# Kernel tuning notes

Hardware: AMD Instinct MI355X
Metric: run time of the kernel (lower is better)

Reference implementation:

```python
import jax, jax.numpy as jnp
import numpy as np

NUM_HEADS = 32
MICRO_BATCHES = 2
TOP_K = 2
LN_EPS = 1e-5


def _mha(x, scale, bias, wq, wk, wv, wo):
    # Pre-LN multi-head self-attention with residual (RealSelfAttention).
    B, S, D = x.shape
    H = NUM_HEADS
    hd = D // H
    res = x
    mu = jnp.mean(x, axis=-1, keepdims=True)
    xc = x - mu
    var = jnp.mean(xc * xc, axis=-1, keepdims=True)
    xn = xc / jnp.sqrt(var + LN_EPS) * scale + bias
    q = (xn @ wq.T).reshape(B, S, H, hd).transpose(0, 2, 1, 3)
    k = (xn @ wk.T).reshape(B, S, H, hd).transpose(0, 2, 1, 3)
    v = (xn @ wv.T).reshape(B, S, H, hd).transpose(0, 2, 1, 3)
    scores = jnp.einsum('bhqd,bhkd->bhqk', q, k) * (1.0 / np.sqrt(hd).astype(np.float32))
    attn = jax.nn.softmax(scores, axis=-1)
    o = jnp.einsum('bhqk,bhkd->bhqd', attn, v).transpose(0, 2, 1, 3).reshape(B, S, D)
    return o @ wo.T + res


def setup_inputs() -> dict:
    key = jax.random.key(0)
    D, E, F = 1024, 8, 4096
    B, S = 4, 1024
    ks = jax.random.split(key, 16)
    w = lambda k, shape: (jax.random.normal(k, shape, dtype=jnp.float32) * 0.02)
    return {
        'x': jax.random.normal(ks[0], (B, S, D), dtype=jnp.float32),
        'ln1_scale': jnp.ones((D,), jnp.float32),
        'ln1_bias': jnp.zeros((D,), jnp.float32),
        'wq1': w(ks[1], (D, D)), 'wk1': w(ks[2], (D, D)),
        'wv1': w(ks[3], (D, D)), 'wo1': w(ks[4], (D, D)),
        'gate_w': w(ks[5], (E, D)),
        'exp_w1': w(ks[6], (E, F, D)), 'exp_b1': jnp.zeros((E, F), jnp.float32),
        'exp_w2': w(ks[7], (E, D, F)), 'exp_b2': jnp.zeros((E, D), jnp.float32),
        'ln2_scale': jnp.ones((D,), jnp.float32),
        'ln2_bias': jnp.zeros((D,), jnp.float32),
        'wq2': w(ks[8], (D, D)), 'wk2': w(ks[9], (D, D)),
        'wv2': w(ks[10], (D, D)), 'wo2': w(ks[11], (D, D)),
    }


def reference(x, ln1_scale, ln1_bias, wq1, wk1, wv1, wo1, gate_w,
              exp_w1, exp_b1, exp_w2, exp_b2,
              ln2_scale, ln2_bias, wq2, wk2, wv2, wo2):
    B, S, D = x.shape
    E = exp_w1.shape[0]
    # PreOps: attention layer L (per-sample, so full-batch apply == per-microbatch apply)
    y = _mha(x, ln1_scale, ln1_bias, wq1, wk1, wv1, wo1)
    # Gate: logits + top-k indices computed in source but never applied to tokens.
    flat = y.reshape(B * S, D)
    logits = flat @ gate_w.T
    _ = jax.lax.top_k(logits, TOP_K)  # indices unused downstream (faithful to source)
    # Dispatch (all_to_all on 1 device == identity): per-microbatch flat tokens are
    # chunked equally across local experts.
    T = (B // MICRO_BATCHES) * S            # tokens per microbatch
    toks = y.reshape(MICRO_BATCHES, E, T // E, D)
    h = jax.nn.gelu(jnp.einsum('metd,efd->metf', toks, exp_w1) + exp_b1[None, :, None, :],
                    approximate=False)
    eo = jnp.einsum('metf,edf->metd', h, exp_w2) + exp_b2[None, :, None, :]
    # Combine (identity) + PostOps: attention layer L+1
    z = eo.reshape(B, S, D)
    out = _mha(z, ln2_scale, ln2_bias, wq2, wk2, wv2, wo2)
    return out
```

## Files before the change

kernel.cpp:

```cpp
#include <hip/hip_runtime.h>

typedef __attribute__((ext_vector_type(8))) short bf16x8;
typedef __attribute__((ext_vector_type(4))) float f32x4;
typedef __attribute__((ext_vector_type(4))) short short4v;

#define DEV __device__ __forceinline__

DEV short f2bf(float f) {
  union { float f; unsigned u; } x; x.f = f;
  unsigned r = x.u + 0x7fffu + ((x.u >> 16) & 1u);
  return (short)(r >> 16);
}

#define GL2LDS16(g, l) __builtin_amdgcn_global_load_lds(                      \
    (const __attribute__((address_space(1))) void*)(g),                       \
    (__attribute__((address_space(3))) void*)(l), 16, 0, 0)

__global__ __launch_bounds__(256) void k_cast_bf16(const float* __restrict__ s,
                                                   short* __restrict__ d, int n4) {
  int i = blockIdx.x * 256 + threadIdx.x;
  if (i >= n4) return;
  float4 v = ((const float4*)s)[i];
  short4v o;
  o[0] = f2bf(v.x); o[1] = f2bf(v.y); o[2] = f2bf(v.z); o[3] = f2bf(v.w);
  ((short4v*)d)[i] = o;
}

__global__ __launch_bounds__(256)
void k_ln(const float* __restrict__ X, const float* __restrict__ G,
          const float* __restrict__ Bi, short* __restrict__ Y) {
  const int row = blockIdx.x, t = threadIdx.x;
  const float4 v = ((const float4*)(X + (size_t)row * 1024))[t];
  float s = v.x + v.y + v.z + v.w;
  float s2 = v.x * v.x + v.y * v.y + v.z * v.z + v.w * v.w;
#pragma unroll
  for (int m = 1; m < 64; m <<= 1) { s += __shfl_xor(s, m); s2 += __shfl_xor(s2, m); }
  __shared__ float rs[4], rq[4];
  const int w = t >> 6, lane = t & 63;
  if (lane == 0) { rs[w] = s; rq[w] = s2; }
  __syncthreads();
  s = rs[0] + rs[1] + rs[2] + rs[3];
  s2 = rq[0] + rq[1] + rq[2] + rq[3];
  const float mu = s * (1.f / 1024.f);
  const float var = s2 * (1.f / 1024.f) - mu * mu;
  const float rstd = rsqrtf(var + 1e-5f);
  const float4 g = ((const float4*)G)[t];
  const float4 bi = ((const float4*)Bi)[t];
  short4v o;
  o[0] = f2bf((v.x - mu) * rstd * g.x + bi.x);
  o[1] = f2bf((v.y - mu) * rstd * g.y + bi.y);
  o[2] = f2bf((v.z - mu) * rstd * g.z + bi.z);
  o[3] = f2bf((v.w - mu) * rstd * g.w + bi.w);
  ((short4v*)(Y + (size_t)row * 1024))[t] = o;
}

template <int EPI, int EXPERT>
__global__ __launch_bounds__(256)
void k_gemm_bt(const short* __restrict__ A, const short* __restrict__ Bt,
               void* __restrict__ Cv, const float* __restrict__ Res,
               const float* __restrict__ Bias, int M, int N, int K) {
  __shared__ __attribute__((aligned(16))) short As[128 * 32];
  __shared__ __attribute__((aligned(16))) short Bs[128 * 32];
  const int tid = threadIdx.x;
  const int w = tid >> 6, lane = tid & 63;
  const int r16 = lane & 15, kg = lane >> 4;
  const int wr = w >> 1, wc = w & 1;

  size_t rowBase = (size_t)blockIdx.y * 128;
  size_t bOff = 0, biasOff = 0;
  if constexpr (EXPERT) {
    int e = blockIdx.z >> 1, mb = blockIdx.z & 1;
    rowBase += (size_t)(mb * 8 + e) * 256;
    bOff = (size_t)e * N * K;
    biasOff = (size_t)e * N;
  }
  const size_t col0 = (size_t)blockIdx.x * 128;
  const short* Ab = A + rowBase * K;
  const short* Bb = Bt + bOff + col0 * K;

  f32x4 acc[4][4] = {};

  for (int k0 = 0; k0 < K; k0 += 32) {
    __syncthreads();
#pragma unroll
    for (int i = 0; i < 2; ++i) {
      int c = (i * 4 + w) * 64 + lane;
      int row = c >> 2;
      int sl = (c & 3) ^ (row & 3);
      GL2LDS16(Ab + (size_t)row * K + k0 + sl * 8, (char*)As + (size_t)(i * 4 + w) * 1024);
      GL2LDS16(Bb + (size_t)row * K + k0 + sl * 8, (char*)Bs + (size_t)(i * 4 + w) * 1024);
    }
    __syncthreads();
    bf16x8 af[4], bg[4];
#pragma unroll
    for (int m = 0; m < 4; ++m) {
      int row = wr * 64 + m * 16 + r16;
      af[m] = *(const bf16x8*)(As + row * 32 + (kg ^ (row & 3)) * 8);
    }
#pragma unroll
    for (int n = 0; n < 4; ++n) {
      int row = wc * 64 + n * 16 + r16;
      bg[n] = *(const bf16x8*)(Bs + row * 32 + (kg ^ (row & 3)) * 8);
    }
#pragma unroll
    for (int m = 0; m < 4; ++m)
#pragma unroll
      for (int n = 0; n < 4; ++n)
        acc[m][n] = __builtin_amdgcn_mfma_f32_16x16x32_bf16(af[m], bg[n], acc[m][n], 0, 0, 0);
  }

#pragma unroll
  for (int m = 0; m < 4; ++m) {
    size_t grow0 = rowBase + wr * 64 + m * 16 + kg * 4;
#pragma unroll
    for (int n = 0; n < 4; ++n) {
      size_t gcol = col0 + wc * 64 + n * 16 + r16;
#pragma unroll
      for (int r = 0; r < 4; ++r) {
        size_t idx = (grow0 + r) * (size_t)N + gcol;
        float v = acc[m][n][r];
        if constexpr (EPI == 1 || EPI == 4) v += Res[idx];
        if constexpr (EPI == 2 || EPI == 3) v += Bias[biasOff + gcol];
        if constexpr (EPI == 2) v = 0.5f * v * (1.f + erff(v * 0.70710678118654752f));
        if constexpr (EPI <= 2) ((short*)Cv)[idx] = f2bf(v);
        else                    ((float*)Cv)[idx] = v;
      }
    }
  }
}

__global__ __launch_bounds__(256, 3)
void k_attn(const short* __restrict__ QKV, short* __restrict__ O) {
  const int qt = blockIdx.x, h = blockIdx.y, b = blockIdx.z;
  const int tid = threadIdx.x, w = tid >> 6, lane = tid & 63;
  const int r16 = lane & 15, kg = lane >> 4;

  __shared__ __attribute__((aligned(16))) short Kl[2][128 * 32];
  __shared__ __attribute__((aligned(16))) short Vt[2][32 * 128];
  __shared__ __attribute__((aligned(16))) short Pl[4][16 * 128];

  const size_t tb = (size_t)b * 1024;
  const int qbase = qt * 128 + w * 32;

  bf16x8 aq[2];
#pragma unroll
  for (int f = 0; f < 2; ++f)
    aq[f] = *(const bf16x8*)(QKV + (tb + qbase + f * 16 + r16) * 3072 + h * 32 + kg * 8);

  f32x4 acc[2][2] = {};
  float lreg[2][4] = {};
  const float scale = 0.17677669529663687f;

  auto stageK = [&](int bid, int kc) {
#pragma unroll
    for (int i = 0; i < 2; ++i) {
      int c = (i * 4 + w) * 64 + lane;
      int row = c >> 2;
      int sl = (c & 3) ^ (row & 3);
      GL2LDS16(QKV + (tb + kc * 128 + row) * 3072 + 1024 + h * 32 + sl * 8,
               (char*)Kl[bid] + (size_t)(i * 4 + w) * 1024);
    }
  };

  stageK(0, 0);
  {
    int c0 = tid,        vr0 = c0 >> 2, d00 = (c0 & 3) * 8;
    int c1 = 256 + tid,  vr1 = c1 >> 2, d01 = (c1 & 3) * 8;
    bf16x8 v0 = *(const bf16x8*)(QKV + (tb + vr0) * 3072 + 2048 + h * 32 + d00);
    bf16x8 v1 = *(const bf16x8*)(QKV + (tb + vr1) * 3072 + 2048 + h * 32 + d01);
#pragma unroll
    for (int j = 0; j < 8; ++j) {
      int da = d00 + j, db = d01 + j;
      Vt[0][((da * 128 + vr0) ^ ((da & 7) << 3))] = v0[j];
      Vt[0][((db * 128 + vr1) ^ ((db & 7) << 3))] = v1[j];
    }
  }
  __syncthreads();

  int bi = 0;
  for (int kc = 0; kc < 8; ++kc) {
    bf16x8 nv0, nv1;
    int nvr0 = 0, nd0 = 0, nvr1 = 0, nd1 = 0;
    if (kc < 7) {
      stageK(bi ^ 1, kc + 1);
      const short* Vg = QKV + (tb + (size_t)(kc + 1) * 128) * 3072 + 2048 + h * 32;
      int c0 = tid;       nvr0 = c0 >> 2; nd0 = (c0 & 3) * 8;
      int c1 = 256 + tid; nvr1 = c1 >> 2; nd1 = (c1 & 3) * 8;
      nv0 = *(const bf16x8*)(Vg + (size_t)nvr0 * 3072 + nd0);
      nv1 = *(const bf16x8*)(Vg + (size_t)nvr1 * 3072 + nd1);
    }

    f32x4 s[2][8];
#pragma unroll
    for (int kt = 0; kt < 8; ++kt) {
      int row = kt * 16 + r16;
      bf16x8 bk = *(const bf16x8*)(Kl[bi] + row * 32 + (kg ^ (row & 3)) * 8);
      f32x4 zz = {0.f, 0.f, 0.f, 0.f};
      s[0][kt] = __builtin_amdgcn_mfma_f32_16x16x32_bf16(aq[0], bk, zz, 0, 0, 0);
      s[1][kt] = __builtin_amdgcn_mfma_f32_16x16x32_bf16(aq[1], bk, zz, 0, 0, 0);
    }

#pragma unroll
    for (int f = 0; f < 2; ++f)
#pragma unroll
      for (int r = 0; r < 4; ++r) {
        float sum = 0.f;
#pragma unroll
        for (int kt = 0; kt < 8; ++kt) {
          float p = __expf(s[f][kt][r] * scale);
          s[f][kt][r] = p;
          sum += p;
        }
#pragma unroll
        for (int m = 1; m < 16; m <<= 1) sum += __shfl_xor(sum, m);
        lreg[f][r] += sum;
      }

    short* P = Pl[w];
#pragma unroll
    for (int f = 0; f < 2; ++f) {
#pragma unroll
      for (int kt = 0; kt < 8; ++kt)
#pragma unroll
        for (int r = 0; r < 4; ++r) {
          int row = kg * 4 + r;
          P[((row * 128 + kt * 16 + r16) ^ ((row & 7) << 3))] = f2bf(s[f][kt][r]);
        }
#pragma unroll
      for (int ks = 0; ks < 4; ++ks) {
        bf16x8 pa = *(const bf16x8*)(P + ((r16 * 128 + ks * 32 + kg * 8) ^ ((r16 & 7) << 3)));
#pragma unroll
        for (int dt = 0; dt < 2; ++dt) {
          int vrow = dt * 16 + r16;
          bf16x8 bv = *(const bf16x8*)(Vt[bi] + ((vrow * 128 + ks * 32 + kg * 8) ^ ((vrow & 7) << 3)));
          acc[f][dt] = __builtin_amdgcn_mfma_f32_16x16x32_bf16(pa, bv, acc[f][dt], 0, 0, 0);
        }
      }
    }

    if (kc < 7) {
#pragma unroll
      for (int j = 0; j < 8; ++j) {
        int da = nd0 + j, db = nd1 + j;
        Vt[bi ^ 1][((da * 128 + nvr0) ^ ((da & 7) << 3))] = nv0[j];
        Vt[bi ^ 1][((db * 128 + nvr1) ^ ((db & 7) << 3))] = nv1[j];
      }
    }

    __syncthreads();
    bi ^= 1;
  }

#pragma unroll
  for (int f = 0; f < 2; ++f)
#pragma unroll
    for (int r = 0; r < 4; ++r) {
      float inv = 1.f / lreg[f][r];
      size_t qrow = tb + qbase + f * 16 + kg * 4 + r;
#pragma unroll
      for (int dt = 0; dt < 2; ++dt)
        O[qrow * 1024 + h * 32 + dt * 16 + r16] = f2bf(acc[f][dt][r] * inv);
    }
}

extern "C" void kernel_launch(void* const* d_in, const int* in_sizes, int n_in,
                              void* d_out, int out_size, void* d_ws, size_t ws_size,
                              hipStream_t stream) {
  const float* x    = (const float*)d_in[0];
  const float* ln1s = (const float*)d_in[1];
  const float* ln1b = (const float*)d_in[2];
  const float* wq1  = (const float*)d_in[3];
  const float* wk1  = (const float*)d_in[4];
  const float* wv1  = (const float*)d_in[5];
  const float* wo1  = (const float*)d_in[6];
  const float* ew1  = (const float*)d_in[8];
  const float* eb1  = (const float*)d_in[9];
  const float* ew2  = (const float*)d_in[10];
  const float* eb2  = (const float*)d_in[11];
  const float* ln2s = (const float*)d_in[12];
  const float* ln2b = (const float*)d_in[13];
  const float* wq2  = (const float*)d_in[14];
  const float* wk2  = (const float*)d_in[15];
  const float* wv2  = (const float*)d_in[16];
  const float* wo2  = (const float*)d_in[17];

  char* ws = (char*)d_ws;
  size_t off = 0;
  auto alloc = [&](size_t bytes) {
    char* p = ws + off;
    off += (bytes + 255) & ~(size_t)255;
    return p;
  };
  short* wqkv1b = (short*)alloc(3072ull * 1024 * 2);
  short* wo1b   = (short*)alloc(1024ull * 1024 * 2);
  short* wqkv2b = (short*)alloc(3072ull * 1024 * 2);
  short* wo2b   = (short*)alloc(1024ull * 1024 * 2);
  short* ew1b   = (short*)alloc(8ull * 4096 * 1024 * 2);
  short* ew2b   = (short*)alloc(8ull * 1024 * 4096 * 2);
  short* xnb    = (short*)alloc(4096ull * 1024 * 2);
  short* qkvo   = (short*)alloc(4096ull * 4096 * 2);
  short* ybf    = (short*)alloc(4096ull * 1024 * 2);
  float* zf     = (float*)alloc(4096ull * 1024 * 4);
  (void)ws_size; (void)in_sizes; (void)n_in; (void)out_size;

  short* QKV = qkvo;
  short* Ob  = qkvo + 4096ull * 3072;
  short* hb  = qkvo;

  auto cast = [&](const float* s, short* d, size_t n) {
    int n4 = (int)(n / 4);
    k_cast_bf16<<<(n4 + 255) / 256, 256, 0, stream>>>(s, d, n4);
  };
  cast(wq1, wqkv1b,           1048576);
  cast(wk1, wqkv1b + 1048576, 1048576);
  cast(wv1, wqkv1b + 2097152, 1048576);
  cast(wo1, wo1b,             1048576);
  cast(wq2, wqkv2b,           1048576);
  cast(wk2, wqkv2b + 1048576, 1048576);
  cast(wv2, wqkv2b + 2097152, 1048576);
  cast(wo2, wo2b,             1048576);
  cast(ew1, ew1b, 8ull * 4096 * 1024);
  cast(ew2, ew2b, 8ull * 1024 * 4096);

  k_ln<<<4096, 256, 0, stream>>>(x, ln1s, ln1b, xnb);
  k_gemm_bt<0, 0><<<dim3(24, 32, 1), 256, 0, stream>>>(xnb, wqkv1b, QKV, nullptr, nullptr, 4096, 3072, 1024);
  k_attn<<<dim3(8, 32, 4), 256, 0, stream>>>(QKV, Ob);
  k_gemm_bt<1, 0><<<dim3(8, 32, 1), 256, 0, stream>>>(Ob, wo1b, ybf, x, nullptr, 4096, 1024, 1024);
  k_gemm_bt<2, 1><<<dim3(32, 2, 16), 256, 0, stream>>>(ybf, ew1b, hb, nullptr, eb1, 256, 4096, 1024);
  k_gemm_bt<3, 1><<<dim3(8, 2, 16), 256, 0, stream>>>(hb, ew2b, zf, nullptr, eb2, 256, 1024, 4096);
  k_ln<<<4096, 256, 0, stream>>>(zf, ln2s, ln2b, xnb);
  k_gemm_bt<0, 0><<<dim3(24, 32, 1), 256, 0, stream>>>(xnb, wqkv2b, QKV, nullptr, nullptr, 4096, 3072, 1024);
  k_attn<<<dim3(8, 32, 4), 256, 0, stream>>>(QKV, Ob);
  k_gemm_bt<4, 0><<<dim3(8, 32, 1), 256, 0, stream>>>(Ob, wo2b, (float*)d_out, zf, nullptr, 4096, 1024, 1024);
}
```

Measured before the change: 609.6 us.

## Double-buffer GEMM LDS tiles and use narrower N tiles for N=1024 GEMMs

```diff
diff --git a/kernel.cpp b/kernel.cpp
--- a/kernel.cpp
+++ b/kernel.cpp
@@ -54,13 +54,15 @@
   ((short4v*)(Y + (size_t)row * 1024))[t] = o;
 }
 
-template <int EPI, int EXPERT>
+template <int EPI, int EXPERT, int BN>
 __global__ __launch_bounds__(256)
 void k_gemm_bt(const short* __restrict__ A, const short* __restrict__ Bt,
                void* __restrict__ Cv, const float* __restrict__ Res,
                const float* __restrict__ Bias, int M, int N, int K) {
-  __shared__ __attribute__((aligned(16))) short As[128 * 32];
-  __shared__ __attribute__((aligned(16))) short Bs[128 * 32];
+  constexpr int NF = BN / 32;
+  constexpr int BR = BN / 64;
+  __shared__ __attribute__((aligned(16))) short As[2][128 * 32];
+  __shared__ __attribute__((aligned(16))) short Bs[2][BN * 32];
   const int tid = threadIdx.x;
   const int w = tid >> 6, lane = tid & 63;
   const int r16 = lane & 15, kg = lane >> 4;
@@ -74,47 +76,60 @@
     bOff = (size_t)e * N * K;
     biasOff = (size_t)e * N;
   }
-  const size_t col0 = (size_t)blockIdx.x * 128;
+  const size_t col0 = (size_t)blockIdx.x * BN;
   const short* Ab = A + rowBase * K;
   const short* Bb = Bt + bOff + col0 * K;
 
-  f32x4 acc[4][4] = {};
-
-  for (int k0 = 0; k0 < K; k0 += 32) {
-    __syncthreads();
+  f32x4 acc[4][NF] = {};
+
+  auto stage = [&](int buf, int k0) {
 #pragma unroll
     for (int i = 0; i < 2; ++i) {
       int c = (i * 4 + w) * 64 + lane;
       int row = c >> 2;
       int sl = (c & 3) ^ (row & 3);
-      GL2LDS16(Ab + (size_t)row * K + k0 + sl * 8, (char*)As + (size_t)(i * 4 + w) * 1024);
-      GL2LDS16(Bb + (size_t)row * K + k0 + sl * 8, (char*)Bs + (size_t)(i * 4 + w) * 1024);
-    }
-    __syncthreads();
-    bf16x8 af[4], bg[4];
+      GL2LDS16(Ab + (size_t)row * K + k0 + sl * 8, (char*)As[buf] + (size_t)(i * 4 + w) * 1024);
+    }
+#pragma unroll
+    for (int i = 0; i < BR; ++i) {
+      int c = (i * 4 + w) * 64 + lane;
+      int row = c >> 2;
+      int sl = (c & 3) ^ (row & 3);
+      GL2LDS16(Bb + (size_t)row * K + k0 + sl * 8, (char*)Bs[buf] + (size_t)(i * 4 + w) * 1024);
+    }
+  };
+
+  stage(0, 0);
+  __syncthreads();
+  int cur = 0;
+  for (int k0 = 0; k0 < K; k0 += 32) {
+    if (k0 + 32 < K) stage(cur ^ 1, k0 + 32);
+    bf16x8 af[4], bg[NF];
 #pragma unroll
     for (int m = 0; m < 4; ++m) {
       int row = wr * 64 + m * 16 + r16;
-      af[m] = *(const bf16x8*)(As + row * 32 + (kg ^ (row & 3)) * 8);
-    }
-#pragma unroll
-    for (int n = 0; n < 4; ++n) {
-      int row = wc * 64 + n * 16 + r16;
-      bg[n] = *(const bf16x8*)(Bs + row * 32 + (kg ^ (row & 3)) * 8);
+      af[m] = *(const bf16x8*)(As[cur] + row * 32 + (kg ^ (row & 3)) * 8);
+    }
+#pragma unroll
+    for (int n = 0; n < NF; ++n) {
+      int row = wc * (BN / 2) + n * 16 + r16;
+      bg[n] = *(const bf16x8*)(Bs[cur] + row * 32 + (kg ^ (row & 3)) * 8);
     }
 #pragma unroll
     for (int m = 0; m < 4; ++m)
 #pragma unroll
-      for (int n = 0; n < 4; ++n)
+      for (int n = 0; n < NF; ++n)
         acc[m][n] = __builtin_amdgcn_mfma_f32_16x16x32_bf16(af[m], bg[n], acc[m][n], 0, 0, 0);
+    __syncthreads();
+    cur ^= 1;
   }
 
 #pragma unroll
   for (int m = 0; m < 4; ++m) {
     size_t grow0 = rowBase + wr * 64 + m * 16 + kg * 4;
 #pragma unroll
-    for (int n = 0; n < 4; ++n) {
-      size_t gcol = col0 + wc * 64 + n * 16 + r16;
+    for (int n = 0; n < NF; ++n) {
+      size_t gcol = col0 + wc * (BN / 2) + n * 16 + r16;
 #pragma unroll
       for (int r = 0; r < 4; ++r) {
         size_t idx = (grow0 + r) * (size_t)N + gcol;
@@ -323,13 +338,13 @@
   cast(ew2, ew2b, 8ull * 1024 * 4096);
 
   k_ln<<<4096, 256, 0, stream>>>(x, ln1s, ln1b, xnb);
-  k_gemm_bt<0, 0><<<dim3(24, 32, 1), 256, 0, stream>>>(xnb, wqkv1b, QKV, nullptr, nullptr, 4096, 3072, 1024);
+  k_gemm_bt<0, 0, 128><<<dim3(24, 32, 1), 256, 0, stream>>>(xnb, wqkv1b, QKV, nullptr, nullptr, 4096, 3072, 1024);
   k_attn<<<dim3(8, 32, 4), 256, 0, stream>>>(QKV, Ob);
-  k_gemm_bt<1, 0><<<dim3(8, 32, 1), 256, 0, stream>>>(Ob, wo1b, ybf, x, nullptr, 4096, 1024, 1024);
-  k_gemm_bt<2, 1><<<dim3(32, 2, 16), 256, 0, stream>>>(ybf, ew1b, hb, nullptr, eb1, 256, 4096, 1024);
-  k_gemm_bt<3, 1><<<dim3(8, 2, 16), 256, 0, stream>>>(hb, ew2b, zf, nullptr, eb2, 256, 1024, 4096);
+  k_gemm_bt<1, 0, 64><<<dim3(16, 32, 1), 256, 0, stream>>>(Ob, wo1b, ybf, x, nullptr, 4096, 1024, 1024);
+  k_gemm_bt<2, 1, 128><<<dim3(32, 2, 16), 256, 0, stream>>>(ybf, ew1b, hb, nullptr, eb1, 256, 4096, 1024);
+  k_gemm_bt<3, 1, 64><<<dim3(16, 2, 16), 256, 0, stream>>>(hb, ew2b, zf, nullptr, eb2, 256, 1024, 4096);
   k_ln<<<4096, 256, 0, stream>>>(zf, ln2s, ln2b, xnb);
-  k_gemm_bt<0, 0><<<dim3(24, 32, 1), 256, 0, stream>>>(xnb, wqkv2b, QKV, nullptr, nullptr, 4096, 3072, 1024);
+  k_gemm_bt<0, 0, 128><<<dim3(24, 32, 1), 256, 0, stream>>>(xnb, wqkv2b, QKV, nullptr, nullptr, 4096, 3072, 1024);
   k_attn<<<dim3(8, 32, 4), 256, 0, stream>>>(QKV, Ob);
-  k_gemm_bt<4, 0><<<dim3(8, 32, 1), 256, 0, stream>>>(Ob, wo2b, (float*)d_out, zf, nullptr, 4096, 1024, 1024);
-}
+  k_gemm_bt<4, 0, 64><<<dim3(16, 32, 1), 256, 0, stream>>>(Ob, wo2b, (float*)d_out, zf, nullptr, 4096, 1024, 1024);
+}
```

New measurement: 574.8 us. -5.7%, faster.
